# Kernel optimization log

Hardware: AMD Instinct MI355X
Metric: run time of the kernel (lower is better)

The kernel has to match this reference:

```python
import jax, jax.numpy as jnp
import numpy as np
from jax.scipy.special import gammaln

REG = 0.1  # reg_param from __init__


def setup_inputs() -> dict:
    key = jax.random.key(0)
    k1, k2 = jax.random.split(key)
    D, C, S, Q = 512, 64, 16, 2048  # feature_dim, n_way, shots, n_query
    X_support = jax.random.normal(k1, (C * S, D), dtype=jnp.float32)
    # balanced class labels (equivalent to argmax of a one-hot y)
    labels = jnp.arange(C * S, dtype=jnp.int32) % C
    X_query = jax.random.normal(k2, (Q, D), dtype=jnp.float32)
    # learned parameters, initialized exactly as in the torch module
    m = jnp.zeros((1, D), dtype=jnp.float32)
    kappa = jnp.asarray(0.1, dtype=jnp.float32)
    nu = jnp.asarray(float(D), dtype=jnp.float32)
    triu_diag = jnp.ones((D,), dtype=jnp.float32)
    triu_lower = jnp.eye(D, dtype=jnp.float32)
    return {"X_support": X_support, "labels": labels, "X_query": X_query,
            "m": m, "kappa": kappa, "nu": nu,
            "triu_diag": triu_diag, "triu_lower": triu_lower, "n_classes": 64}


def _forward(X_support, X_query, m, kappa, nu, triu_diag, triu_lower, labels, n_classes):
    N, D = X_support.shape
    C = int(n_classes)
    S = N // C  # balanced episode: N_j == S for every class

    # lower_triu = diag(|triu_diag|) + triu_lower * strictly_lower_mask
    mask = jnp.tril(jnp.ones((D, D), dtype=X_support.dtype), -1)
    L = jnp.diag(jnp.abs(triu_diag)) + triu_lower * mask

    kap = jnp.abs(kappa) + 1e-6
    nu_ = jnp.clip(nu, D - 1 + 1e-6)

    # group support samples by class: [C, S, D] (stable sort keeps per-class order)
    order = jnp.argsort(labels)
    Xg = X_support[order].reshape(C, S, D)
    Xmean = Xg.mean(axis=1)  # [C, D]

    # posterior means mu_j = kappa/(kappa+N) m + N/(kappa+N) mean(X_j)
    mu = (kap / (kap + S)) * m + (S / (kap + S)) * Xmean  # [C, D]

    # sum_outer(X_j) as one batched GEMM instead of a per-row loop
    XtX = jnp.einsum('csd,cse->cde', Xg, Xg)  # [C, D, D]
    base = L @ L.T + kap * (m.T @ m)          # [D, D], shared across classes
    S_ns = base[None] + XtX - (kap + S) * jnp.einsum('cd,ce->cde', mu, mu)
    sigma = S_ns * ((kap + S + 1.0) / ((nu_ + S - D + 1.0) * (kap + S)))  # [C, D, D]

    eye = jnp.eye(D, dtype=sigma.dtype)
    sigma_inv = (1.0 - REG) * jnp.linalg.inv(sigma) + REG * eye  # regularize()

    common = nu_ + S + 1.0 - D  # scalar (equal shots per class)
    _, logdet = jnp.linalg.slogdet(sigma)  # [C]
    bias = (gammaln(0.5 * (common + D)) - gammaln(0.5 * common)
            - 0.5 * D * jnp.log(common) - 0.5 * logdet)  # [C]

    # batched Mahalanobis distances: replaces nested python loops in predict()
    diff = X_query[None, :, :] - mu[:, None, :]              # [C, Q, D]
    t = jnp.einsum('cqd,cde->cqe', diff, sigma_inv)          # [C, Q, D]
    dist = jnp.sum(t * diff, axis=-1)                        # [C, Q]

    logits = bias[:, None] - 0.5 * (common + D) * jnp.log1p(dist / common)
    return logits.T  # [Q, C]


def reference(X_support, labels, X_query, m, kappa, nu, triu_diag, triu_lower, n_classes):
    return _forward(X_support, X_query, m, kappa, nu, triu_diag, triu_lower,
                    labels, n_classes)
```

## Files before the change

kernel.cpp:

```cpp
#include <hip/hip_runtime.h>
#include <math.h>

#define DD    512
#define CNUM  64
#define SHOTS 16
#define NSUP  1024
#define QNQ   2048
#define REGP  0.1f
#define XKS   4

typedef __attribute__((ext_vector_type(8))) short short8;
typedef __attribute__((ext_vector_type(4))) float f32x4;

__device__ __forceinline__ unsigned short f2bf(float f) {
  unsigned int u = __float_as_uint(f);
  unsigned int r = (u + 0x7fffu + ((u >> 16) & 1u)) >> 16;
  return (unsigned short)r;
}
__device__ __forceinline__ float bf2f(unsigned short h) {
  return __uint_as_float((unsigned int)h << 16);
}

static constexpr size_t OFF_W     = 0;
static constexpr size_t OFF_MU    = OFF_W     + 512*512;
static constexpr size_t OFF_Y     = OFF_MU    + 64*512;
static constexpr size_t OFF_Z     = OFF_Y     + 3136*512;
static constexpr size_t OFF_WM    = OFF_Z     + 3136;
static constexpr size_t OFF_CONST = OFF_WM    + 512;
static constexpr size_t OFF_IDX   = OFF_CONST + 16;
static constexpr size_t OFF_RMAP  = OFF_IDX   + 1024;
static constexpr size_t OFF_ZG    = OFF_RMAP  + 1088;
static constexpr size_t OFF_VMU   = OFF_ZG    + 1088;
static constexpr size_t OFF_MUBMU = OFF_VMU   + 1088;
static constexpr size_t OFF_MUN   = OFF_MUBMU + 64;
static constexpr size_t OFF_MINV  = OFF_MUN   + 64;
static constexpr size_t OFF_BIAS  = OFF_MINV  + 64*289;
static constexpr size_t OFF_QNRM  = OFF_BIAS  + 64;
static constexpr size_t OFF_YN    = OFF_QNRM  + 2048;
static constexpr size_t OFF_XMU   = OFF_YN    + 2048;
static constexpr size_t OFF_RG    = OFF_XMU   + (size_t)XKS*2048*64;
static constexpr size_t OFF_P     = OFF_RG    + 1088*2048;
static constexpr size_t OFF_PX    = OFF_P     + 3136*512;
static constexpr size_t OFF_PW    = OFF_PX    + 3136*512;


__global__ __launch_bounds__(256) void f_init(const float* tdiag, const float* tlow,
    const float* kappa, const float* nu, const int* labels, const float* Xs,
    const float* Xq, const float* m, float* W, float* cst, int* idx,
    int* rowmap, float* mu, float* mun,
    unsigned short* PX, unsigned short* PW) {
  __shared__ float sh[2 * 64 * 68 + 32 * 33];
  __shared__ int sidx[SHOTS];
  int b = blockIdx.x, tid = threadIdx.x;
  if (b == 0) {
    if (tid == 0) {
      float kap = fabsf(kappa[0]) + 1e-6f;
      float nu_ = fmaxf(nu[0], (float)(DD - 1) + 1e-6f);
      float common = nu_ + (float)SHOTS + 1.0f - (float)DD;
      float scale = (kap + SHOTS + 1.0f) / ((nu_ + SHOTS - DD + 1.0f) * (kap + SHOTS));
      cst[0] = kap;
      cst[1] = scale;
      cst[2] = common;
      cst[3] = 0.5f * (common + DD);
      cst[4] = lgammaf(0.5f * (common + DD)) - lgammaf(0.5f * common)
               - 0.5f * (float)DD * logf(common);
      cst[5] = -(kap + SHOTS);
      cst[6] = kap / (kap + SHOTS);
      cst[7] = 1.0f / (kap + SHOTS);
      cst[8] = (float)DD * logf(scale);
      cst[9] = -1.0f / (kap + SHOTS);
    }
  } else if (b < 65) {
    int c = b - 1;
    if (tid < 64) {
      int lane = tid, cnt = 0;
      for (int i0 = 0; i0 < NSUP; i0 += 64) {
        int lab = labels[i0 + lane];
        unsigned long long mm = __ballot(lab == c);
        if (lab == c) {
          int pos = cnt + __popcll(mm & ((1ull << lane) - 1ull));
          if (pos < SHOTS) idx[c * SHOTS + pos] = i0 + lane;
        }
        cnt += __popcll(mm);
      }
    }
    __syncthreads();
    if (tid < 17)
      rowmap[c * 17 + tid] = (tid < SHOTS) ? (QNQ + idx[c * SHOTS + tid])
                                           : (QNQ + NSUP + c);
  } else if (b < 129) {
    int c = b - 65;
    if (tid < 64) {
      int lane = tid, cnt = 0;
      for (int i0 = 0; i0 < NSUP; i0 += 64) {
        int lab = labels[i0 + lane];
        unsigned long long mm = __ballot(lab == c);
        if (lab == c) {
          int pos = cnt + __popcll(mm & ((1ull << lane) - 1ull));
          if (pos < SHOTS) sidx[pos] = i0 + lane;
        }
        cnt += __popcll(mm);
      }
    }
    __syncthreads();
    float kap = fabsf(kappa[0]) + 1e-6f;
    float cm = kap / (kap + SHOTS), cx = 1.0f / (kap + SHOTS);
    float* red = sh;
    float acc = 0.0f;
    size_t prow = (size_t)(3072 + c) * 1024;
    for (int d = tid; d < DD; d += 256) {
      float s = 0.0f;
      for (int sh_ = 0; sh_ < SHOTS; sh_++)
        s += Xs[(size_t)sidx[sh_] * DD + d];
      float v = cm * m[d] + cx * s;
      mu[(size_t)c * DD + d] = v;
      unsigned short h = f2bf(v), l = f2bf(v - bf2f(h));
      PX[prow + d] = h;
      PX[prow + 512 + d] = l;
      acc += v * v;
    }
    red[tid] = acc;
    __syncthreads();
    for (int off = 128; off > 0; off >>= 1) {
      if (tid < off) red[tid] += red[tid + off];
      __syncthreads();
    }
    if (tid == 0) mun[c] = red[0];
  } else if (b < 137) {
    int jb = b - 129;
    float* Ld = sh;
    float* Wd = sh + 64 * 68;
    float* tsh = sh + 2 * 64 * 68;
    for (int t = tid; t < 4096; t += 256) {
      int r = t >> 6, c = t & 63;
      int gr = jb * 64 + r;
      float v = (r == c) ? fabsf(tdiag[gr])
              : (r > c ? tlow[(size_t)gr * DD + jb * 64 + c] : 0.0f);
      Ld[r * 68 + c] = v;
      Wd[r * 68 + c] = 0.0f;
    }
    __syncthreads();
    if (tid < 64) {
      int s = tid >> 4, t = tid & 15;
      int r0 = s * 16;
      #pragma unroll
      for (int i = 0; i < 16; i++) {
        float w = (i == t) ? 1.0f : 0.0f;
        #pragma unroll
        for (int k = 0; k < 16; k++)
          if (k < i) w -= Ld[(r0 + i) * 68 + r0 + k] * Wd[(r0 + k) * 68 + r0 + t];
        Wd[(r0 + i) * 68 + r0 + t] = w / Ld[(r0 + i) * 68 + r0 + i];
      }
    }
    __syncthreads();
    for (int g2 = 0; g2 < 2; g2++) {
      int r0 = g2 * 32 + 16, c0 = g2 * 32;
      int rr = tid >> 4, cc = tid & 15;
      float t_ = 0.0f;
      #pragma unroll
      for (int k = 0; k < 16; k++)
        t_ += Ld[(r0 + rr) * 68 + c0 + k] * Wd[(c0 + k) * 68 + c0 + cc];
      tsh[rr * 33 + cc] = t_;
      __syncthreads();
      float x = 0.0f;
      #pragma unroll
      for (int k = 0; k < 16; k++)
        x -= Wd[(r0 + rr) * 68 + r0 + k] * tsh[k * 33 + cc];
      Wd[(r0 + rr) * 68 + c0 + cc] = x;
      __syncthreads();
    }
    {
      int rr = tid >> 6, cc = tid & 63;
      #pragma unroll
      for (int p = 0; p < 4; p++) {
        int r = rr + p * 4, c = cc;
        if (c < 32) {
          float t_ = 0.0f;
          #pragma unroll
          for (int k = 0; k < 32; k++)
            t_ += Ld[(32 + r) * 68 + k] * Wd[k * 68 + c];
          tsh[r * 33 + c] = t_;
        } else {
          int c2 = c - 32;
          float t_ = 0.0f;
          #pragma unroll
          for (int k = 0; k < 32; k++)
            t_ += Ld[(32 + r + 16) * 68 + k] * Wd[k * 68 + c2];
          tsh[(r + 16) * 33 + c2] = t_;
        }
      }
      __syncthreads();
      #pragma unroll
      for (int p = 0; p < 4; p++) {
        int r = rr + p * 4, c = cc;
        int r2 = (c < 32) ? r : r + 16;
        int c2 = (c < 32) ? c : c - 32;
        float x = 0.0f;
        #pragma unroll
        for (int k = 0; k < 32; k++)
          x -= Wd[(32 + r2) * 68 + 32 + k] * tsh[k * 33 + c2];
        Wd[(32 + r2) * 68 + c2] = x;
      }
    }
    __syncthreads();
    float* Wblk = W + (size_t)(jb * 64) * DD + jb * 64;
    for (int t = tid; t < 4096; t += 256) {
      int r = t >> 6, c = t & 63;
      float v = Wd[r * 68 + c];
      Wblk[(size_t)r * DD + c] = v;
      unsigned short h = f2bf(v), l = f2bf(v - bf2f(h));
      size_t prow = (size_t)(jb * 64 + r) * 1024 + jb * 64 + c;
      PW[prow] = h;
      PW[prow + 512] = l;
    }
  } else {
    int r0 = (b - 137) * 4;
    int row = r0 + (tid >> 6), lane = tid & 63;
    const float* src = (row < QNQ) ? Xq + (size_t)row * DD
                                   : Xs + (size_t)(row - QNQ) * DD;
    size_t prow = (size_t)row * 1024;
    #pragma unroll
    for (int p = 0; p < 2; p++) {
      int col = lane * 8 + p * 4;
      float4 v = *(const float4*)(src + col);
      ushort4 hi, lo;
      hi.x = f2bf(v.x); lo.x = f2bf(v.x - bf2f(hi.x));
      hi.y = f2bf(v.y); lo.y = f2bf(v.y - bf2f(hi.y));
      hi.z = f2bf(v.z); lo.z = f2bf(v.z - bf2f(hi.z));
      hi.w = f2bf(v.w); lo.w = f2bf(v.w - bf2f(hi.w));
      *(ushort4*)(PX + prow + col) = hi;
      *(ushort4*)(PX + prow + 512 + col) = lo;
    }
  }
}

__device__ __forceinline__ void tile_stage(float* S, const float* __restrict__ G, int ldg) {
  int tid = threadIdx.x;
  #pragma unroll
  for (int p = 0; p < 4; p++) {
    int f4 = tid + 256 * p;
    int row = f4 >> 4, c4 = (f4 & 15) * 4;
    *(float4*)&S[row * 68 + c4] = *(const float4*)(G + (size_t)row * ldg + c4);
  }
}
__device__ __forceinline__ void tile_fma(float acc[4][4], const float* As, const float* Bs) {
  int tid = threadIdx.x, tr = tid >> 4, tc = tid & 15;
  #pragma unroll
  for (int kk = 0; kk < 64; kk++) {
    float a[4];
    #pragma unroll
    for (int x = 0; x < 4; x++) a[x] = As[(tr * 4 + x) * 68 + kk];
    float4 bv = *(const float4*)&Bs[kk * 68 + tc * 4];
    float bb[4] = {bv.x, bv.y, bv.z, bv.w};
    #pragma unroll
    for (int x = 0; x < 4; x++)
      #pragma unroll
      for (int y = 0; y < 4; y++) acc[x][y] += a[x] * bb[y];
  }
}
__device__ __forceinline__ void tile_out_neg(const float acc[4][4], float* W,
    unsigned short* PW, int gr0, int gc0) {
  int tid = threadIdx.x, tr = tid >> 4, tc = tid & 15;
  #pragma unroll
  for (int x = 0; x < 4; x++) {
    #pragma unroll
    for (int y = 0; y < 4; y++) {
      float v = -acc[x][y];
      W[(size_t)(gr0 + tr * 4 + x) * DD + gc0 + tc * 4 + y] = v;
      unsigned short h = f2bf(v), l = f2bf(v - bf2f(h));
      size_t prow = (size_t)(gr0 + tr * 4 + x) * 1024 + gc0 + tc * 4 + y;
      PW[prow] = h;
      PW[prow + 512] = l;
    }
  }
}

#define GBK 16
__global__ __launch_bounds__(256) void k_m128_xmu(const float* __restrict__ tlow,
    const float* __restrict__ W_, float* __restrict__ Wout,
    const float* __restrict__ Xq, const float* __restrict__ Mu,
    float* __restrict__ xmup, unsigned short* __restrict__ PW) {
  __shared__ float sh[3 * 64 * 68];
  int b = blockIdx.x, tid = threadIdx.x;
  if (b < 4) {
    float* As = sh;
    float* Bs = sh + 64 * 68;
    float* tsh = sh + 2 * 64 * 68;
    int base = b * 128;
    float tacc[4][4] = {};
    tile_stage(As, tlow + (size_t)(base + 64) * DD + base, DD);
    tile_stage(Bs, W_ + (size_t)base * DD + base, DD);
    __syncthreads();
    tile_fma(tacc, As, Bs);
    __syncthreads();
    {
      int tr = tid >> 4, tc = tid & 15;
      #pragma unroll
      for (int x = 0; x < 4; x++)
        #pragma unroll
        for (int y = 0; y < 4; y++) tsh[(tr * 4 + x) * 68 + tc * 4 + y] = tacc[x][y];
    }
    tile_stage(As, W_ + (size_t)(base + 64) * DD + base + 64, DD);
    __syncthreads();
    float xacc[4][4] = {};
    tile_fma(xacc, As, tsh);
    tile_out_neg(xacc, Wout, PW, base + 64, base);
  } else {
    float* Ms = sh;
    float* Qs = sh + 64 * 68;
    int xb = b - 4;
    int bm = (xb & 63) * 32, kq = xb >> 6;
    int tr = tid >> 4, tc = tid & 15;
    float acc[4][2] = {};
    int k0s = kq * (DD / XKS), k0e = k0s + DD / XKS;
    for (int k0 = k0s; k0 < k0e; k0 += GBK) {
      {
        int row = tid >> 2, k4 = tid & 3;
        float4 v = *(const float4*)(Mu + (size_t)row * DD + k0 + k4 * 4);
        Ms[(k4 * 4 + 0) * 68 + row] = v.x; Ms[(k4 * 4 + 1) * 68 + row] = v.y;
        Ms[(k4 * 4 + 2) * 68 + row] = v.z; Ms[(k4 * 4 + 3) * 68 + row] = v.w;
      }
      if (tid < 128) {
        int row = tid >> 2, k4 = tid & 3;
        float4 v = *(const float4*)(Xq + (size_t)(bm + row) * DD + k0 + k4 * 4);
        Qs[(k4 * 4 + 0) * 36 + row] = v.x; Qs[(k4 * 4 + 1) * 36 + row] = v.y;
        Qs[(k4 * 4 + 2) * 36 + row] = v.z; Qs[(k4 * 4 + 3) * 36 + row] = v.w;
      }
      __syncthreads();
      #pragma unroll
      for (int kk = 0; kk < GBK; kk++) {
        float4 m0 = *(const float4*)&Ms[kk * 68 + tr * 4];
        float a[4] = {m0.x, m0.y, m0.z, m0.w};
        float q0 = Qs[kk * 36 + tc * 2], q1 = Qs[kk * 36 + tc * 2 + 1];
        #pragma unroll
        for (int y = 0; y < 4; y++) {
          acc[y][0] += a[y] * q0;
          acc[y][1] += a[y] * q1;
        }
      }
      __syncthreads();
    }
    #pragma unroll
    for (int y = 0; y < 4; y++) {
      float2 v = make_float2(acc[y][0], acc[y][1]);
      *(float2*)(xmup + ((size_t)kq * CNUM + tr * 4 + y) * QNQ + bm + tc * 2) = v;
    }
  }
}

__global__ __launch_bounds__(256) void k_m256(const float* __restrict__ tlow,
    float* __restrict__ W, unsigned short* __restrict__ PW) {
  __shared__ float sh[3 * 64 * 68];
  float* As = sh;
  float* Bs = sh + 64 * 68;
  float* tsh = sh + 2 * 64 * 68;
  int b = blockIdx.x, tid = threadIdx.x;
  int g = b >> 2, rem = b & 3, i = rem >> 1, j = rem & 1;
  int base = g * 256;
  float xacc[4][4] = {};
  for (int k = 0; k <= i; k++) {
    float tacc[4][4] = {};
    for (int l = j; l < 2; l++) {
      __syncthreads();
      tile_stage(As, tlow + (size_t)(base + 128 + 64 * k) * DD + base + 64 * l, DD);
      tile_stage(Bs, W + (size_t)(base + 64 * l) * DD + base + 64 * j, DD);
      __syncthreads();
      tile_fma(tacc, As, Bs);
    }
    __syncthreads();
    {
      int tr = tid >> 4, tc = tid & 15;
      #pragma unroll
      for (int x = 0; x < 4; x++)
        #pragma unroll
        for (int y = 0; y < 4; y++) tsh[(tr * 4 + x) * 68 + tc * 4 + y] = tacc[x][y];
    }
    tile_stage(As, W + (size_t)(base + 128 + 64 * i) * DD + base + 128 + 64 * k, DD);
    __syncthreads();
    tile_fma(xacc, As, tsh);
  }
  tile_out_neg(xacc, W, PW, base + 128 + 64 * i, base + 64 * j);
}

__device__ __forceinline__ void nn64_sh(float* As, float* Bs,
    const float* __restrict__ A, int lda, const float* __restrict__ B, int ldb,
    float* __restrict__ Cd, int ldc, int k0, int k1, float sgn,
    unsigned short* __restrict__ Pw, int gr0, int gc0) {
  int tid = threadIdx.x, tr = tid >> 4, tc = tid & 15;
  float acc[4][4] = {};
  for (int kc = k0; kc < k1; kc += 64) {
    #pragma unroll
    for (int p = 0; p < 4; p++) {
      int f4 = tid + 256 * p;
      int row = f4 >> 4, c4 = f4 & 15;
      *(float4*)&As[row * 68 + c4 * 4] = *(const float4*)(A + (size_t)row * lda + kc + c4 * 4);
      *(float4*)&Bs[row * 68 + c4 * 4] = *(const float4*)(B + (size_t)(kc + row) * ldb + c4 * 4);
    }
    __syncthreads();
    #pragma unroll
    for (int kk = 0; kk < 64; kk++) {
      float a[4];
      #pragma unroll
      for (int x = 0; x < 4; x++) a[x] = As[(tr * 4 + x) * 68 + kk];
      float4 bv = *(const float4*)&Bs[kk * 68 + tc * 4];
      float bb[4] = {bv.x, bv.y, bv.z, bv.w};
      #pragma unroll
      for (int x = 0; x < 4; x++)
        #pragma unroll
        for (int y = 0; y < 4; y++) acc[x][y] += a[x] * bb[y];
    }
    __syncthreads();
  }
  #pragma unroll
  for (int x = 0; x < 4; x++) {
    float4 v = make_float4(sgn * acc[x][0], sgn * acc[x][1],
                           sgn * acc[x][2], sgn * acc[x][3]);
    *(float4*)(Cd + (size_t)(tr * 4 + x) * ldc + tc * 4) = v;
    if (Pw) {
      size_t prow = (size_t)(gr0 + tr * 4 + x) * 1024 + gc0 + tc * 4;
      float vv[4] = {v.x, v.y, v.z, v.w};
      #pragma unroll
      for (int y = 0; y < 4; y++) {
        unsigned short h = f2bf(vv[y]), l = f2bf(vv[y] - bf2f(h));
        Pw[prow + y] = h;
        Pw[prow + 512 + y] = l;
      }
    }
  }
}

__global__ __launch_bounds__(256) void k_triT(const float* __restrict__ tlow,
                                              const float* __restrict__ W,
                                              float* __restrict__ T, int s) {
  __shared__ float sh[2 * 64 * 68];
  int h = s >> 1, tiles = h >> 6, per = tiles * tiles;
  int g = blockIdx.x / per, rem = blockIdx.x % per;
  int ti = rem / tiles, tj = rem % tiles;
  int base = g * s;
  const float* A = tlow + (size_t)(base + h + ti * 64) * DD + base;
  const float* B = W + (size_t)base * DD + base + tj * 64;
  float* Cd = T + (size_t)g * h * h + (size_t)(ti * 64) * h + tj * 64;
  nn64_sh(sh, sh + 64 * 68, A, DD, B, DD, Cd, h, tj * 64, h, 1.0f, nullptr, 0, 0);
}

__global__ __launch_bounds__(256) void k_triX(float* __restrict__ W,
                                              const float* __restrict__ T, int s,
                                              unsigned short* __restrict__ PW) {
  __shared__ float sh[2 * 64 * 68];
  int h = s >> 1, tiles = h >> 6, per = tiles * tiles;
  int g = blockIdx.x / per, rem = blockIdx.x % per;
  int ti = rem / tiles, tj = rem % tiles;
  int base = g * s;
  const float* A = W + (size_t)(base + h + ti * 64) * DD + base + h;
  const float* B = T + (size_t)g * h * h + tj * 64;
  int gr0 = base + h + ti * 64, gc0 = base + tj * 64;
  float* Cd = W + (size_t)gr0 * DD + gc0;
  nn64_sh(sh, sh + 64 * 68, A, DD, B, h, Cd, DD, 0, (ti + 1) * 64, -1.0f, PW, gr0, gc0);
}

#define PSTR 80
__global__ __launch_bounds__(256) void f_y_wm(const unsigned short* __restrict__ PX,
    const unsigned short* __restrict__ PW, const float* __restrict__ W,
    const float* __restrict__ m, float* __restrict__ Y,
    unsigned short* __restrict__ Pm, float* __restrict__ wm) {
  __shared__ unsigned short AshH[64 * PSTR];
  __shared__ unsigned short AshL[64 * PSTR];
  __shared__ unsigned short BshH[64 * PSTR];
  __shared__ unsigned short BshL[64 * PSTR];
  int b = blockIdx.x, tid = threadIdx.x;
  if (b < 392) {
    int mt = b >> 3, nt = b & 7;
    int bm = mt * 64, bn = nt * 64;
    int lane = tid & 63, wave = tid >> 6;
    int wr = wave >> 1, wc = wave & 1;
    int mrow = lane & 15, q = lane >> 4;
    f32x4 acc00 = {}, acc01 = {}, acc10 = {}, acc11 = {};
    int kchunks = nt + 1;
    for (int it = 0; it < kchunks; it++) {
      int kc = it * 64;
      #pragma unroll
      for (int p = 0; p < 2; p++) {
        int idx = tid + 256 * p;
        int row = idx >> 3, c8 = (idx & 7) * 8;
        *(short8*)&AshH[row * PSTR + c8] =
            *(const short8*)(PX + (size_t)(bm + row) * 1024 + kc + c8);
        *(short8*)&AshL[row * PSTR + c8] =
            *(const short8*)(PX + (size_t)(bm + row) * 1024 + 512 + kc + c8);
        *(short8*)&BshH[row * PSTR + c8] =
            *(const short8*)(PW + (size_t)(bn + row) * 1024 + kc + c8);
        *(short8*)&BshL[row * PSTR + c8] =
            *(const short8*)(PW + (size_t)(bn + row) * 1024 + 512 + kc + c8);
      }
      __syncthreads();
      #pragma unroll
      for (int ks = 0; ks < 2; ks++) {
        int ko = ks * 32 + q * 8;
        short8 ah0 = *(const short8*)&AshH[(wr * 32 + mrow) * PSTR + ko];
        short8 ah1 = *(const short8*)&AshH[(wr * 32 + 16 + mrow) * PSTR + ko];
        short8 al0 = *(const short8*)&AshL[(wr * 32 + mrow) * PSTR + ko];
        short8 al1 = *(const short8*)&AshL[(wr * 32 + 16 + mrow) * PSTR + ko];
        short8 bh0 = *(const short8*)&BshH[(wc * 32 + mrow) * PSTR + ko];
        short8 bh1 = *(const short8*)&BshH[(wc * 32 + 16 + mrow) * PSTR + ko];
        short8 bl0 = *(const short8*)&BshL[(wc * 32 + mrow) * PSTR + ko];
        short8 bl1 = *(const short8*)&BshL[(wc * 32 + 16 + mrow) * PSTR + ko];
        acc00 = __builtin_amdgcn_mfma_f32_16x16x32_bf16(ah0, bh0, acc00, 0, 0, 0);
        acc00 = __builtin_amdgcn_mfma_f32_16x16x32_bf16(ah0, bl0, acc00, 0, 0, 0);
        acc00 = __builtin_amdgcn_mfma_f32_16x16x32_bf16(al0, bh0, acc00, 0, 0, 0);
        acc00 = __builtin_amdgcn_mfma_f32_16x16x32_bf16(al0, bl0, acc00, 0, 0, 0);
        acc01 = __builtin_amdgcn_mfma_f32_16x16x32_bf16(ah0, bh1, acc01, 0, 0, 0);
        acc01 = __builtin_amdgcn_mfma_f32_16x16x32_bf16(ah0, bl1, acc01, 0, 0, 0);
        acc01 = __builtin_amdgcn_mfma_f32_16x16x32_bf16(al0, bh1, acc01, 0, 0, 0);
        acc01 = __builtin_amdgcn_mfma_f32_16x16x32_bf16(al0, bl1, acc01, 0, 0, 0);
        acc10 = __builtin_amdgcn_mfma_f32_16x16x32_bf16(ah1, bh0, acc10, 0, 0, 0);
        acc10 = __builtin_amdgcn_mfma_f32_16x16x32_bf16(ah1, bl0, acc10, 0, 0, 0);
        acc10 = __builtin_amdgcn_mfma_f32_16x16x32_bf16(al1, bh0, acc10, 0, 0, 0);
        acc10 = __builtin_amdgcn_mfma_f32_16x16x32_bf16(al1, bl0, acc10, 0, 0, 0);
        acc11 = __builtin_amdgcn_mfma_f32_16x16x32_bf16(ah1, bh1, acc11, 0, 0, 0);
        acc11 = __builtin_amdgcn_mfma_f32_16x16x32_bf16(ah1, bl1, acc11, 0, 0, 0);
        acc11 = __builtin_amdgcn_mfma_f32_16x16x32_bf16(al1, bh1, acc11, 0, 0, 0);
        acc11 = __builtin_amdgcn_mfma_f32_16x16x32_bf16(al1, bl1, acc11, 0, 0, 0);
      }
      __syncthreads();
    }
    #pragma unroll
    for (int r = 0; r < 4; r++) {
      int row0 = bm + wr * 32 + q * 4 + r;
      int row1 = row0 + 16;
      int col0 = bn + wc * 32 + mrow;
      float vv[4] = {acc00[r], acc01[r], acc10[r], acc11[r]};
      int rows[4] = {row0, row0, row1, row1};
      int cols[4] = {col0, col0 + 16, col0, col0 + 16};
      #pragma unroll
      for (int e = 0; e < 4; e++) {
        Y[(size_t)rows[e] * DD + cols[e]] = vv[e];
        unsigned short h = f2bf(vv[e]), l = f2bf(vv[e] - bf2f(h));
        Pm[(size_t)rows[e] * 1024 + cols[e]] = h;
        Pm[(size_t)rows[e] * 1024 + 512 + cols[e]] = l;
      }
    }
  } else {
    int wave = tid >> 6, lane = tid & 63;
    int row = (b - 392) * 4 + wave;
    float s = 0.0f;
    for (int j = lane; j <= row; j += 64) s += W[(size_t)row * DD + j] * m[j];
    for (int off = 32; off > 0; off >>= 1) s += __shfl_down(s, off);
    if (lane == 0) wm[row] = s;
  }
}

__global__ __launch_bounds__(256) void f_z_rg_gram(const unsigned short* __restrict__ Pm,
    const float* __restrict__ Y, const float* __restrict__ tdiag,
    const int* __restrict__ rowmap, const float* __restrict__ Xq,
    const float* __restrict__ wm, float* __restrict__ cst,
    float* __restrict__ Rg,
    float* __restrict__ z, float* __restrict__ qn, float* __restrict__ yn,
    float* __restrict__ zg, float* __restrict__ Vmu, float* __restrict__ muBmu,
    float* __restrict__ Minv, float* __restrict__ bias) {
  __shared__ float sh[9920];
  __shared__ float csmS;
  int b = blockIdx.x, tid = threadIdx.x;
  if (b < 64) {
    int c = b;
    int lane = tid & 63, wave = tid >> 6;
    float* Ys  = sh;
    float* aug = sh + 8772;
    float* zsv = aug + 306;
    float kap = cst[0], cst9 = cst[9];
    for (int t = tid; t < 17 * 128; t += 256) {
      int r = t >> 7, col = t & 127;
      *(float4*)&Ys[r * 516 + col * 4] =
          *(const float4*)(Y + (size_t)rowmap[c * 17 + r] * DD + col * 4);
    }
    float ldb_r = 0.0f;
    if (wave == 0) {
      float aa = 0.0f, ll = 0.0f;
      for (int t = lane; t < DD; t += 64) {
        float w = wm[t]; aa += w * w;
        ll += logf(fabsf(tdiag[t]));
      }
      #pragma unroll
      for (int off = 32; off > 0; off >>= 1) {
        aa += __shfl_xor(aa, off);
        ll += __shfl_xor(ll, off);
      }
      ldb_r = 2.0f * ll + logf(1.0f + kap * aa);
      if (lane == 0) csmS = kap / (1.0f + kap * aa);
    }
    __syncthreads();
    if (wave > 0) {
      for (int a = wave - 1; a < 17; a += 3) {
        float s = 0.0f;
        for (int j = lane; j < 128; j += 64) {
          float4 yv = *(const float4*)&Ys[a * 516 + j * 4];
          float4 wv = *(const float4*)(wm + j * 4);
          s += yv.x * wv.x + yv.y * wv.y + yv.z * wv.z + yv.w * wv.w;
        }
        #pragma unroll
        for (int off = 32; off > 0; off >>= 1) s += __shfl_xor(s, off);
        if (lane == 0) zsv[a] = s;
      }
    }
    __syncthreads();
    float csm = csmS;
    for (int e = tid; e < 153; e += 256) {
      int a = (int)((sqrtf(8.0f * (float)e + 1.0f) - 1.0f) * 0.5f);
      while (((a + 1) * (a + 2)) / 2 <= e) a++;
      while ((a * (a + 1)) / 2 > e) a--;
      int bb = e - (a * (a + 1)) / 2;
      const float* ra = &Ys[a * 516];
      const float* rb = &Ys[bb * 516];
      float s = 0.0f;
      for (int k = 0; k < 128; k++) {
        float4 va = *(const float4*)&ra[k * 4];
        float4 vb = *(const float4*)&rb[k * 4];
        s += va.x * vb.x + va.y * vb.y + va.z * vb.z + va.w * vb.w;
      }
      float g = s - csm * zsv[a] * zsv[bb];
      if (a == bb) g += (a < 16) ? 1.0f : cst9;
      aug[a * 18 + bb] = g;
      if (a != bb) aug[bb * 18 + a] = g;
    }
    __syncthreads();
    if (wave == 0) {
      float colv[17];
      bool left = lane < 17;
      bool right = (lane >= 17 && lane < 34);
      #pragma unroll
      for (int r = 0; r < 17; r++) {
        float lv = aug[r * 18 + (lane & 31)];
        colv[r] = left ? lv : ((right && (lane - 17) == r) ? 1.0f : 0.0f);
      }
      float det = 0.0f;
      #pragma unroll
      for (int k = 0; k < 17; k++) {
        float best = fabsf(colv[k]); int bp = k;
        #pragma unroll
        for (int r = k + 1; r < 17; r++) {
          float v = fabsf(colv[r]);
          if (v > best) { best = v; bp = r; }
        }
        int p = __shfl(bp, k);
        float pv = colv[k];
        #pragma unroll
        for (int r = k + 1; r < 17; r++) pv = (p == r) ? colv[r] : pv;
        float oldk = colv[k];
        #pragma unroll
        for (int r = k + 1; r < 17; r++) colv[r] = (p == r) ? oldk : colv[r];
        colv[k] = pv;
        float piv = __shfl(pv, k);
        if (lane == 0) det += logf(fabsf(piv));
        float invp = 1.0f / piv;
        float rk = pv * invp;
        colv[k] = rk;
        #pragma unroll
        for (int r = 0; r < 17; r++) {
          if (r == k) continue;
          float ck = __shfl(colv[r], k);
          colv[r] = fmaf(-ck, rk, colv[r]);
        }
      }
      if (right) {
        int bb = lane - 17;
        #pragma unroll
        for (int r = 0; r < 17; r++)
          Minv[(size_t)c * 289 + r * 17 + bb] = colv[r];
      }
      if (lane == 0) {
        float slog = logf(fabsf(cst[5])) + det;
        float logdetSigma = cst[8] + ldb_r + slog;
        bias[c] = cst[4] - 0.5f * logdetSigma;
      }
    } else if (wave == 1) {
      if (lane < 17) {
        float gv = aug[lane * 18 + 16];
        if (lane == 16) gv -= cst9;
        Vmu[c * 17 + lane] = gv;
        if (lane == 16) muBmu[c] = gv;
        zg[c * 17 + lane] = zsv[lane];
      }
    }
  } else if (b == 64) {
    if (tid < 64) {
      float aa = 0.0f, ll = 0.0f;
      for (int t = tid; t < DD; t += 64) {
        float w = wm[t]; aa += w * w;
        ll += logf(fabsf(tdiag[t]));
      }
      #pragma unroll
      for (int off = 32; off > 0; off >>= 1) {
        aa += __shfl_xor(aa, off);
        ll += __shfl_xor(ll, off);
      }
      if (tid == 0) {
        float kap = cst[0];
        cst[10] = kap / (1.0f + kap * aa);
        cst[11] = 2.0f * ll + logf(1.0f + kap * aa);
      }
    }
  } else if (b < 609) {
    unsigned short* ush = (unsigned short*)sh;
    unsigned short* Ash = ush;
    unsigned short* Bsh = ush + 64 * PSTR;
    unsigned short* Csh = ush + 2 * 64 * PSTR;
    int rb = b - 65;
    int bm = (rb >> 5) * 64, bn = (rb & 31) * 64;
    int lane = tid & 63, wave = tid >> 6;
    int wr = wave >> 1, wc = wave & 1;
    int mrow = lane & 15, q = lane >> 4;
    int srowA[2];
    #pragma unroll
    for (int p = 0; p < 2; p++) srowA[p] = rowmap[bm + ((tid + 256 * p) >> 3)];
    f32x4 acc00 = {}, acc01 = {}, acc10 = {}, acc11 = {};
    for (int it = 0; it < 16; it++) {
      int kc = it * 64;
      int kcX = kc ^ 512;
      #pragma unroll
      for (int p = 0; p < 2; p++) {
        int idx = tid + 256 * p;
        int row = idx >> 3, c8 = (idx & 7) * 8;
        *(short8*)&Ash[row * PSTR + c8] =
            *(const short8*)(Pm + (size_t)srowA[p] * 1024 + kc + c8);
        *(short8*)&Bsh[row * PSTR + c8] =
            *(const short8*)(Pm + (size_t)(bn + row) * 1024 + kc + c8);
        *(short8*)&Csh[row * PSTR + c8] =
            *(const short8*)(Pm + (size_t)(bn + row) * 1024 + kcX + c8);
      }
      __syncthreads();
      #pragma unroll
      for (int ks = 0; ks < 2; ks++) {
        int ko = ks * 32 + q * 8;
        short8 a0 = *(const short8*)&Ash[(wr * 32 + mrow) * PSTR + ko];
        short8 a1 = *(const short8*)&Ash[(wr * 32 + 16 + mrow) * PSTR + ko];
        short8 b0 = *(const short8*)&Bsh[(wc * 32 + mrow) * PSTR + ko];
        short8 b1 = *(const short8*)&Bsh[(wc * 32 + 16 + mrow) * PSTR + ko];
        short8 c0 = *(const short8*)&Csh[(wc * 32 + mrow) * PSTR + ko];
        short8 c1 = *(const short8*)&Csh[(wc * 32 + 16 + mrow) * PSTR + ko];
        acc00 = __builtin_amdgcn_mfma_f32_16x16x32_bf16(a0, b0, acc00, 0, 0, 0);
        acc01 = __builtin_amdgcn_mfma_f32_16x16x32_bf16(a0, b1, acc01, 0, 0, 0);
        acc10 = __builtin_amdgcn_mfma_f32_16x16x32_bf16(a1, b0, acc10, 0, 0, 0);
        acc11 = __builtin_amdgcn_mfma_f32_16x16x32_bf16(a1, b1, acc11, 0, 0, 0);
        acc00 = __builtin_amdgcn_mfma_f32_16x16x32_bf16(a0, c0, acc00, 0, 0, 0);
        acc01 = __builtin_amdgcn_mfma_f32_16x16x32_bf16(a0, c1, acc01, 0, 0, 0);
        acc10 = __builtin_amdgcn_mfma_f32_16x16x32_bf16(a1, c0, acc10, 0, 0, 0);
        acc11 = __builtin_amdgcn_mfma_f32_16x16x32_bf16(a1, c1, acc11, 0, 0, 0);
      }
      __syncthreads();
    }
    #pragma unroll
    for (int r = 0; r < 4; r++) {
      int row0 = bm + wr * 32 + q * 4 + r;
      int row1 = row0 + 16;
      int col0 = bn + wc * 32 + mrow;
      Rg[(size_t)row0 * QNQ + col0]      = acc00[r];
      Rg[(size_t)row0 * QNQ + col0 + 16] = acc01[r];
      Rg[(size_t)row1 * QNQ + col0]      = acc10[r];
      Rg[(size_t)row1 * QNQ + col0 + 16] = acc11[r];
    }
  } else {
    int wave = tid >> 6, lane = tid & 63;
    int row = (b - 609) * 4 + wave;
    const float* xr = Xq + (size_t)row * DD;
    const float* yr = Y + (size_t)row * DD;
    float sz = 0.0f, s1 = 0.0f, s2 = 0.0f;
    for (int j4 = lane; j4 < 128; j4 += 64) {
      float4 xv = *(const float4*)(xr + j4 * 4);
      float4 yv = *(const float4*)(yr + j4 * 4);
      float4 wv = *(const float4*)(wm + j4 * 4);
      sz += yv.x * wv.x + yv.y * wv.y + yv.z * wv.z + yv.w * wv.w;
      s1 += xv.x * xv.x + xv.y * xv.y + xv.z * xv.z + xv.w * xv.w;
      s2 += yv.x * yv.x + yv.y * yv.y + yv.z * yv.z + yv.w * yv.w;
    }
    for (int off = 32; off > 0; off >>= 1) {
      sz += __shfl_down(sz, off);
      s1 += __shfl_down(s1, off);
      s2 += __shfl_down(s2, off);
    }
    if (lane == 0) {
      z[row] = sz;
      qn[row] = s1;
      yn[row] = s2;
    }
  }
}

__global__ __launch_bounds__(256) void k_logits(const float* __restrict__ Rg,
    const float* z, const float* zg,
    const float* Vmu, const float* muBmu, const float* mun, const float* yn,
    const float* qn, const float* xmup, const float* Minv, const float* bias,
    const float* cst, float* out) {
  __shared__ float Ms[289], Vs[17], Zs[17];
  int c = blockIdx.y;
  int q = blockIdx.x * 256 + threadIdx.x;
  for (int t = threadIdx.x; t < 289; t += 256) Ms[t] = Minv[(size_t)c * 289 + t];
  if (threadIdx.x < 17) {
    Vs[threadIdx.x] = Vmu[c * 17 + threadIdx.x];
    Zs[threadIdx.x] = zg[c * 17 + threadIdx.x];
  }
  __syncthreads();
  float csm = cst[10], scale = cst[1], common = cst[2], coef = cst[3];
  float zq = z[q];
  float r[17];
  float xBmu = 0.0f;
  for (int a = 0; a < 17; a++) {
    float raw = Rg[(size_t)(c * 17 + a) * QNQ + q] - csm * Zs[a] * zq;
    if (a == 16) xBmu = raw;
    r[a] = raw - Vs[a];
  }
  float qB = yn[q] - csm * zq * zq;
  float quadB = qB - 2.0f * xBmu + muBmu[c];
  float corr = 0.0f;
  for (int a = 0; a < 17; a++) {
    float e = 0.0f;
    for (int bb = 0; bb < 17; bb++) e += Ms[a * 17 + bb] * r[bb];
    corr += r[a] * e;
  }
  float distB = (quadB - corr) / scale;
  float xm = 0.0f;
  #pragma unroll
  for (int p = 0; p < XKS; p++)
    xm += xmup[((size_t)(p * CNUM + c)) * QNQ + q];
  float dn = qn[q] - 2.0f * xm + mun[c];
  float dist = (1.0f - REGP) * distB + REGP * dn;
  out[(size_t)q * CNUM + c] = bias[c] - coef * log1pf(dist / common);
}

extern "C" void kernel_launch(void* const* d_in, const int* in_sizes, int n_in,
                              void* d_out, int out_size, void* d_ws, size_t ws_size,
                              hipStream_t stream) {
  const float* Xs    = (const float*)d_in[0];
  const int*   labels= (const int*)d_in[1];
  const float* Xq    = (const float*)d_in[2];
  const float* m     = (const float*)d_in[3];
  const float* kappa = (const float*)d_in[4];
  const float* nu    = (const float*)d_in[5];
  const float* tdiag = (const float*)d_in[6];
  const float* tlow  = (const float*)d_in[7];
  float* ws = (float*)d_ws;
  float* W    = ws + OFF_W;
  float* mu   = ws + OFF_MU;
  float* Y    = ws + OFF_Y;
  float* z    = ws + OFF_Z;
  float* wm   = ws + OFF_WM;
  float* cst  = ws + OFF_CONST;
  int*   idx  = (int*)(ws + OFF_IDX);
  int*   rmap = (int*)(ws + OFF_RMAP);
  float* zg   = ws + OFF_ZG;
  float* Vmu  = ws + OFF_VMU;
  float* muBmu= ws + OFF_MUBMU;
  float* mun  = ws + OFF_MUN;
  float* Minv = ws + OFF_MINV;
  float* bias = ws + OFF_BIAS;
  float* qn   = ws + OFF_QNRM;
  float* yn   = ws + OFF_YN;
  float* xmup = ws + OFF_XMU;
  float* Rg   = ws + OFF_RG;
  unsigned short* P  = (unsigned short*)(ws + OFF_P);
  unsigned short* PX = (unsigned short*)(ws + OFF_PX);
  unsigned short* PW = (unsigned short*)(ws + OFF_PW);
  float* Ttmp = ws + OFF_RG;
  float* out  = (float*)d_out;

  f_init<<<905, 256, 0, stream>>>(tdiag, tlow, kappa, nu, labels, Xs, Xq, m,
                                  W, cst, idx, rmap, mu, mun, PX, PW);
  k_m128_xmu<<<260, 256, 0, stream>>>(tlow, W, W, Xq, mu, xmup, PW);
  k_m256<<<8, 256, 0, stream>>>(tlow, W, PW);
  k_triT<<<16, 256, 0, stream>>>(tlow, W, Ttmp, 512);
  k_triX<<<16, 256, 0, stream>>>(W, Ttmp, 512, PW);
  f_y_wm<<<520, 256, 0, stream>>>(PX, PW, W, m, Y, P, wm);
  f_z_rg_gram<<<64 + 1 + 544 + 512, 256, 0, stream>>>(P, Y, tdiag, rmap, Xq, wm,
                                                      cst, Rg, z, qn, yn,
                                                      zg, Vmu, muBmu, Minv, bias);
  k_logits<<<dim3(QNQ / 256, CNUM), 256, 0, stream>>>(Rg, z, zg, Vmu, muBmu,
                                                      mun, yn, qn, xmup, Minv, bias,
                                                      cst, out);
  (void)in_sizes; (void)n_in; (void)out_size; (void)ws_size;
}
```

Measured before the change: 189.1 us.

## Fuse triangular-inverse stages and Y GEMM into one kernel with atomic flag dependencies

Merges five separate launches (k_m128_xmu, k_m256, k_triT, k_triX, f_y_wm) into a single kernel, k_mid. Its block ranges wait on global atomic counters for the blocks they depend on instead of relying on kernel boundaries. This removes launch gaps and lets independent work (the xmu GEMM, the Y tiles on the first half of W, and the wm rows) overlap with the serial triangular-inverse chain. The risk is deadlock if waiting blocks get scheduled ahead of producer blocks and fill the GPU, and there is extra polling overhead. Flags are reset in f_init block 0 on each run.

```diff
diff --git a/kernel.cpp b/kernel.cpp
--- a/kernel.cpp
+++ b/kernel.cpp
@@ -42,17 +42,34 @@
 static constexpr size_t OFF_P     = OFF_RG    + 1088*2048;
 static constexpr size_t OFF_PX    = OFF_P     + 3136*512;
 static constexpr size_t OFF_PW    = OFF_PX    + 3136*512;
-
+static constexpr size_t OFF_FLAGS = OFF_PW    + 512*1024/2;
+
+
+__device__ __forceinline__ void flag_signal(int* f) {
+  __syncthreads();
+  __builtin_amdgcn_fence(__ATOMIC_RELEASE, "agent");
+  if (threadIdx.x == 0)
+    __hip_atomic_fetch_add(f, 1, __ATOMIC_RELAXED, __HIP_MEMORY_SCOPE_AGENT);
+}
+__device__ __forceinline__ void flag_wait(int* f, int n) {
+  if (threadIdx.x == 0) {
+    while (__hip_atomic_load(f, __ATOMIC_RELAXED, __HIP_MEMORY_SCOPE_AGENT) < n)
+      __builtin_amdgcn_s_sleep(2);
+  }
+  __syncthreads();
+  __builtin_amdgcn_fence(__ATOMIC_ACQUIRE, "agent");
+}
 
 __global__ __launch_bounds__(256) void f_init(const float* tdiag, const float* tlow,
     const float* kappa, const float* nu, const int* labels, const float* Xs,
     const float* Xq, const float* m, float* W, float* cst, int* idx,
     int* rowmap, float* mu, float* mun,
-    unsigned short* PX, unsigned short* PW) {
+    unsigned short* PX, unsigned short* PW, int* flags) {
   __shared__ float sh[2 * 64 * 68 + 32 * 33];
   __shared__ int sidx[SHOTS];
   int b = blockIdx.x, tid = threadIdx.x;
   if (b == 0) {
+    if (tid < 8) flags[tid] = 0;
     if (tid == 0) {
       float kap = fabsf(kappa[0]) + 1e-6f;
       float nu_ = fmaxf(nu[0], (float)(DD - 1) + 1e-6f);
@@ -275,21 +292,72 @@
   }
 }
 
+__device__ __forceinline__ void nn64_sh(float* As, float* Bs,
+    const float* __restrict__ A, int lda, const float* __restrict__ B, int ldb,
+    float* __restrict__ Cd, int ldc, int k0, int k1, float sgn,
+    unsigned short* __restrict__ Pw, int gr0, int gc0) {
+  int tid = threadIdx.x, tr = tid >> 4, tc = tid & 15;
+  float acc[4][4] = {};
+  for (int kc = k0; kc < k1; kc += 64) {
+    #pragma unroll
+    for (int p = 0; p < 4; p++) {
+      int f4 = tid + 256 * p;
+      int row = f4 >> 4, c4 = f4 & 15;
+      *(float4*)&As[row * 68 + c4 * 4] = *(const float4*)(A + (size_t)row * lda + kc + c4 * 4);
+      *(float4*)&Bs[row * 68 + c4 * 4] = *(const float4*)(B + (size_t)(kc + row) * ldb + c4 * 4);
+    }
+    __syncthreads();
+    #pragma unroll
+    for (int kk = 0; kk < 64; kk++) {
+      float a[4];
+      #pragma unroll
+      for (int x = 0; x < 4; x++) a[x] = As[(tr * 4 + x) * 68 + kk];
+      float4 bv = *(const float4*)&Bs[kk * 68 + tc * 4];
+      float bb[4] = {bv.x, bv.y, bv.z, bv.w};
+      #pragma unroll
+      for (int x = 0; x < 4; x++)
+        #pragma unroll
+        for (int y = 0; y < 4; y++) acc[x][y] += a[x] * bb[y];
+    }
+    __syncthreads();
+  }
+  #pragma unroll
+  for (int x = 0; x < 4; x++) {
+    float4 v = make_float4(sgn * acc[x][0], sgn * acc[x][1],
+                           sgn * acc[x][2], sgn * acc[x][3]);
+    *(float4*)(Cd + (size_t)(tr * 4 + x) * ldc + tc * 4) = v;
+    if (Pw) {
+      size_t prow = (size_t)(gr0 + tr * 4 + x) * 1024 + gc0 + tc * 4;
+      float vv[4] = {v.x, v.y, v.z, v.w};
+      #pragma unroll
+      for (int y = 0; y < 4; y++) {
+        unsigned short h = f2bf(vv[y]), l = f2bf(vv[y] - bf2f(h));
+        Pw[prow + y] = h;
+        Pw[prow + 512 + y] = l;
+      }
+    }
+  }
+}
+
 #define GBK 16
-__global__ __launch_bounds__(256) void k_m128_xmu(const float* __restrict__ tlow,
-    const float* __restrict__ W_, float* __restrict__ Wout,
-    const float* __restrict__ Xq, const float* __restrict__ Mu,
-    float* __restrict__ xmup, unsigned short* __restrict__ PW) {
-  __shared__ float sh[3 * 64 * 68];
+#define PSTR 80
+
+__global__ __launch_bounds__(256, 4) void k_mid(const float* __restrict__ tlow,
+    float* __restrict__ W, const float* __restrict__ Xq,
+    const float* __restrict__ Mu, float* __restrict__ xmup,
+    unsigned short* __restrict__ PW, const unsigned short* __restrict__ PX,
+    const float* __restrict__ m, float* __restrict__ Y,
+    unsigned short* __restrict__ Pm, float* __restrict__ wm,
+    float* __restrict__ T, int* flags) {
+  __shared__ float sh[10240];
   int b = blockIdx.x, tid = threadIdx.x;
   if (b < 4) {
     float* As = sh;
     float* Bs = sh + 64 * 68;
-    float* tsh = sh + 2 * 64 * 68;
     int base = b * 128;
     float tacc[4][4] = {};
     tile_stage(As, tlow + (size_t)(base + 64) * DD + base, DD);
-    tile_stage(Bs, W_ + (size_t)base * DD + base, DD);
+    tile_stage(Bs, W + (size_t)base * DD + base, DD);
     __syncthreads();
     tile_fma(tacc, As, Bs);
     __syncthreads();
@@ -298,17 +366,66 @@
       #pragma unroll
       for (int x = 0; x < 4; x++)
         #pragma unroll
-        for (int y = 0; y < 4; y++) tsh[(tr * 4 + x) * 68 + tc * 4 + y] = tacc[x][y];
-    }
-    tile_stage(As, W_ + (size_t)(base + 64) * DD + base + 64, DD);
+        for (int y = 0; y < 4; y++) Bs[(tr * 4 + x) * 68 + tc * 4 + y] = tacc[x][y];
+    }
+    tile_stage(As, W + (size_t)(base + 64) * DD + base + 64, DD);
     __syncthreads();
     float xacc[4][4] = {};
-    tile_fma(xacc, As, tsh);
-    tile_out_neg(xacc, Wout, PW, base + 64, base);
-  } else {
+    tile_fma(xacc, As, Bs);
+    tile_out_neg(xacc, W, PW, base + 64, base);
+    flag_signal(flags + 0);
+  } else if (b < 12) {
+    flag_wait(flags + 0, 4);
+    float* As = sh;
+    float* Bs = sh + 64 * 68;
+    int rb = b - 4;
+    int g = rb >> 2, rem = rb & 3, i = rem >> 1, j = rem & 1;
+    int base = g * 256;
+    float xacc[4][4] = {};
+    for (int k = 0; k <= i; k++) {
+      float tacc[4][4] = {};
+      for (int l = j; l < 2; l++) {
+        __syncthreads();
+        tile_stage(As, tlow + (size_t)(base + 128 + 64 * k) * DD + base + 64 * l, DD);
+        tile_stage(Bs, W + (size_t)(base + 64 * l) * DD + base + 64 * j, DD);
+        __syncthreads();
+        tile_fma(tacc, As, Bs);
+      }
+      __syncthreads();
+      {
+        int tr = tid >> 4, tc = tid & 15;
+        #pragma unroll
+        for (int x = 0; x < 4; x++)
+          #pragma unroll
+          for (int y = 0; y < 4; y++) Bs[(tr * 4 + x) * 68 + tc * 4 + y] = tacc[x][y];
+      }
+      tile_stage(As, W + (size_t)(base + 128 + 64 * i) * DD + base + 128 + 64 * k, DD);
+      __syncthreads();
+      tile_fma(xacc, As, Bs);
+    }
+    tile_out_neg(xacc, W, PW, base + 128 + 64 * i, base + 64 * j);
+    flag_signal(flags + 1);
+  } else if (b < 28) {
+    flag_wait(flags + 1, 8);
+    int rem = b - 12, ti = rem >> 2, tj = rem & 3;
+    const float* A = tlow + (size_t)(256 + ti * 64) * DD;
+    const float* B = W + (size_t)tj * 64;
+    float* Cd = T + (size_t)(ti * 64) * 256 + tj * 64;
+    nn64_sh(sh, sh + 64 * 68, A, DD, B, DD, Cd, 256, tj * 64, 256, 1.0f, nullptr, 0, 0);
+    flag_signal(flags + 2);
+  } else if (b < 44) {
+    flag_wait(flags + 2, 16);
+    int rem = b - 28, ti = rem >> 2, tj = rem & 3;
+    const float* A = W + (size_t)(256 + ti * 64) * DD + 256;
+    const float* B = T + tj * 64;
+    int gr0 = 256 + ti * 64, gc0 = tj * 64;
+    float* Cd = W + (size_t)gr0 * DD + gc0;
+    nn64_sh(sh, sh + 64 * 68, A, DD, B, 256, Cd, DD, 0, (ti + 1) * 64, -1.0f, PW, gr0, gc0);
+    flag_signal(flags + 3);
+  } else if (b < 300) {
     float* Ms = sh;
     float* Qs = sh + 64 * 68;
-    int xb = b - 4;
+    int xb = b - 44;
     int bm = (xb & 63) * 32, kq = xb >> 6;
     int tr = tid >> 4, tc = tid & 15;
     float acc[4][2] = {};
@@ -345,131 +462,21 @@
       float2 v = make_float2(acc[y][0], acc[y][1]);
       *(float2*)(xmup + ((size_t)kq * CNUM + tr * 4 + y) * QNQ + bm + tc * 2) = v;
     }
-  }
-}
-
-__global__ __launch_bounds__(256) void k_m256(const float* __restrict__ tlow,
-    float* __restrict__ W, unsigned short* __restrict__ PW) {
-  __shared__ float sh[3 * 64 * 68];
-  float* As = sh;
-  float* Bs = sh + 64 * 68;
-  float* tsh = sh + 2 * 64 * 68;
-  int b = blockIdx.x, tid = threadIdx.x;
-  int g = b >> 2, rem = b & 3, i = rem >> 1, j = rem & 1;
-  int base = g * 256;
-  float xacc[4][4] = {};
-  for (int k = 0; k <= i; k++) {
-    float tacc[4][4] = {};
-    for (int l = j; l < 2; l++) {
-      __syncthreads();
-      tile_stage(As, tlow + (size_t)(base + 128 + 64 * k) * DD + base + 64 * l, DD);
-      tile_stage(Bs, W + (size_t)(base + 64 * l) * DD + base + 64 * j, DD);
-      __syncthreads();
-      tile_fma(tacc, As, Bs);
-    }
-    __syncthreads();
-    {
-      int tr = tid >> 4, tc = tid & 15;
-      #pragma unroll
-      for (int x = 0; x < 4; x++)
-        #pragma unroll
-        for (int y = 0; y < 4; y++) tsh[(tr * 4 + x) * 68 + tc * 4 + y] = tacc[x][y];
-    }
-    tile_stage(As, W + (size_t)(base + 128 + 64 * i) * DD + base + 128 + 64 * k, DD);
-    __syncthreads();
-    tile_fma(xacc, As, tsh);
-  }
-  tile_out_neg(xacc, W, PW, base + 128 + 64 * i, base + 64 * j);
-}
-
-__device__ __forceinline__ void nn64_sh(float* As, float* Bs,
-    const float* __restrict__ A, int lda, const float* __restrict__ B, int ldb,
-    float* __restrict__ Cd, int ldc, int k0, int k1, float sgn,
-    unsigned short* __restrict__ Pw, int gr0, int gc0) {
-  int tid = threadIdx.x, tr = tid >> 4, tc = tid & 15;
-  float acc[4][4] = {};
-  for (int kc = k0; kc < k1; kc += 64) {
-    #pragma unroll
-    for (int p = 0; p < 4; p++) {
-      int f4 = tid + 256 * p;
-      int row = f4 >> 4, c4 = f4 & 15;
-      *(float4*)&As[row * 68 + c4 * 4] = *(const float4*)(A + (size_t)row * lda + kc + c4 * 4);
-      *(float4*)&Bs[row * 68 + c4 * 4] = *(const float4*)(B + (size_t)(kc + row) * ldb + c4 * 4);
-    }
-    __syncthreads();
-    #pragma unroll
-    for (int kk = 0; kk < 64; kk++) {
-      float a[4];
-      #pragma unroll
-      for (int x = 0; x < 4; x++) a[x] = As[(tr * 4 + x) * 68 + kk];
-      float4 bv = *(const float4*)&Bs[kk * 68 + tc * 4];
-      float bb[4] = {bv.x, bv.y, bv.z, bv.w};
-      #pragma unroll
-      for (int x = 0; x < 4; x++)
-        #pragma unroll
-        for (int y = 0; y < 4; y++) acc[x][y] += a[x] * bb[y];
-    }
-    __syncthreads();
-  }
-  #pragma unroll
-  for (int x = 0; x < 4; x++) {
-    float4 v = make_float4(sgn * acc[x][0], sgn * acc[x][1],
-                           sgn * acc[x][2], sgn * acc[x][3]);
-    *(float4*)(Cd + (size_t)(tr * 4 + x) * ldc + tc * 4) = v;
-    if (Pw) {
-      size_t prow = (size_t)(gr0 + tr * 4 + x) * 1024 + gc0 + tc * 4;
-      float vv[4] = {v.x, v.y, v.z, v.w};
-      #pragma unroll
-      for (int y = 0; y < 4; y++) {
-        unsigned short h = f2bf(vv[y]), l = f2bf(vv[y] - bf2f(h));
-        Pw[prow + y] = h;
-        Pw[prow + 512 + y] = l;
-      }
-    }
-  }
-}
-
-__global__ __launch_bounds__(256) void k_triT(const float* __restrict__ tlow,
-                                              const float* __restrict__ W,
-                                              float* __restrict__ T, int s) {
-  __shared__ float sh[2 * 64 * 68];
-  int h = s >> 1, tiles = h >> 6, per = tiles * tiles;
-  int g = blockIdx.x / per, rem = blockIdx.x % per;
-  int ti = rem / tiles, tj = rem % tiles;
-  int base = g * s;
-  const float* A = tlow + (size_t)(base + h + ti * 64) * DD + base;
-  const float* B = W + (size_t)base * DD + base + tj * 64;
-  float* Cd = T + (size_t)g * h * h + (size_t)(ti * 64) * h + tj * 64;
-  nn64_sh(sh, sh + 64 * 68, A, DD, B, DD, Cd, h, tj * 64, h, 1.0f, nullptr, 0, 0);
-}
-
-__global__ __launch_bounds__(256) void k_triX(float* __restrict__ W,
-                                              const float* __restrict__ T, int s,
-                                              unsigned short* __restrict__ PW) {
-  __shared__ float sh[2 * 64 * 68];
-  int h = s >> 1, tiles = h >> 6, per = tiles * tiles;
-  int g = blockIdx.x / per, rem = blockIdx.x % per;
-  int ti = rem / tiles, tj = rem % tiles;
-  int base = g * s;
-  const float* A = W + (size_t)(base + h + ti * 64) * DD + base + h;
-  const float* B = T + (size_t)g * h * h + tj * 64;
-  int gr0 = base + h + ti * 64, gc0 = base + tj * 64;
-  float* Cd = W + (size_t)gr0 * DD + gc0;
-  nn64_sh(sh, sh + 64 * 68, A, DD, B, h, Cd, DD, 0, (ti + 1) * 64, -1.0f, PW, gr0, gc0);
-}
-
-#define PSTR 80
-__global__ __launch_bounds__(256) void f_y_wm(const unsigned short* __restrict__ PX,
-    const unsigned short* __restrict__ PW, const float* __restrict__ W,
-    const float* __restrict__ m, float* __restrict__ Y,
-    unsigned short* __restrict__ Pm, float* __restrict__ wm) {
-  __shared__ unsigned short AshH[64 * PSTR];
-  __shared__ unsigned short AshL[64 * PSTR];
-  __shared__ unsigned short BshH[64 * PSTR];
-  __shared__ unsigned short BshL[64 * PSTR];
-  int b = blockIdx.x, tid = threadIdx.x;
-  if (b < 392) {
-    int mt = b >> 3, nt = b & 7;
+  } else if (b < 692) {
+    int t = b - 300, mt, nt;
+    if (t < 196) {
+      mt = t >> 2; nt = t & 3;
+      flag_wait(flags + 1, 8);
+    } else {
+      int u = t - 196;
+      mt = u >> 2; nt = 4 + (u & 3);
+      flag_wait(flags + 3, 16);
+    }
+    unsigned short* ush = (unsigned short*)sh;
+    unsigned short* AshH = ush;
+    unsigned short* AshL = ush + 64 * PSTR;
+    unsigned short* BshH = ush + 2 * 64 * PSTR;
+    unsigned short* BshL = ush + 3 * 64 * PSTR;
     int bm = mt * 64, bn = nt * 64;
     int lane = tid & 63, wave = tid >> 6;
     int wr = wave >> 1, wc = wave & 1;
@@ -539,8 +546,11 @@
       }
     }
   } else {
+    int w = b - 692;
+    if (w < 64) flag_wait(flags + 1, 8);
+    else       flag_wait(flags + 3, 16);
     int wave = tid >> 6, lane = tid & 63;
-    int row = (b - 392) * 4 + wave;
+    int row = w * 4 + wave;
     float s = 0.0f;
     for (int j = lane; j <= row; j += 64) s += W[(size_t)row * DD + j] * m[j];
     for (int off = 32; off > 0; off >>= 1) s += __shfl_down(s, off);
@@ -857,16 +867,14 @@
   unsigned short* P  = (unsigned short*)(ws + OFF_P);
   unsigned short* PX = (unsigned short*)(ws + OFF_PX);
   unsigned short* PW = (unsigned short*)(ws + OFF_PW);
+  int*   flags = (int*)(ws + OFF_FLAGS);
   float* Ttmp = ws + OFF_RG;
   float* out  = (float*)d_out;
 
   f_init<<<905, 256, 0, stream>>>(tdiag, tlow, kappa, nu, labels, Xs, Xq, m,
-                                  W, cst, idx, rmap, mu, mun, PX, PW);
-  k_m128_xmu<<<260, 256, 0, stream>>>(tlow, W, W, Xq, mu, xmup, PW);
-  k_m256<<<8, 256, 0, stream>>>(tlow, W, PW);
-  k_triT<<<16, 256, 0, stream>>>(tlow, W, Ttmp, 512);
-  k_triX<<<16, 256, 0, stream>>>(W, Ttmp, 512, PW);
-  f_y_wm<<<520, 256, 0, stream>>>(PX, PW, W, m, Y, P, wm);
+                                  W, cst, idx, rmap, mu, mun, PX, PW, flags);
+  k_mid<<<820, 256, 0, stream>>>(tlow, W, Xq, mu, xmup, PW, PX, m, Y, P, wm,
+                                 Ttmp, flags);
   f_z_rg_gram<<<64 + 1 + 544 + 512, 256, 0, stream>>>(P, Y, tdiag, rmap, Xq, wm,
                                                       cst, Rg, z, qn, yn,
                                                       zg, Vmu, muBmu, Minv, bias);
```

Result: slower. 207.3 us (+9.7%).
